# Optimization experiments

Measured on AMD Instinct MI355X. Metric: run time of the kernel, lower is better.

Reference implementation:

```python
import math
import jax, jax.numpy as jnp
import numpy as np

TOPK = 10
GAMMA = 0.0
DELTA = 0.05
EPS = 1e-8
QR_RANK_EPS = 1e-6
B, D, C = 4096, 2048, 10000


def setup_inputs() -> dict:
    key = jax.random.key(0)
    kz, kw, kn = jax.random.split(key, 3)
    z = jax.random.normal(kz, (B, D), jnp.float32)
    W = jax.random.normal(kw, (C, D), jnp.float32) * 0.02
    logits = z @ W.T                      # (B, C)
    y = jnp.argmax(logits, axis=1)        # correct-class labels -> positive margins
    noise = jax.random.normal(kn, (B, D), jnp.float32)  # one Gaussian draw per sample
    return {"z": z, "y": y, "logits": logits, "W": W, "noise": noise}


def reference(z, y, logits, W, noise):
    # z: (B,D), y: (B,), logits: (B,C), W: (C,D), noise: (B,D)
    b, d = z.shape
    c = W.shape[0]
    k = min(TOPK, c - 1)
    log_term = math.log(1.0 / max(DELTA, 1e-12))

    # top-K confusing classes (exclude true class)
    lm = logits.at[jnp.arange(b), y].set(-1e9)
    _, topk_idx = jax.lax.top_k(lm, k)            # (B, K)

    w_y = W[y]                                    # (B, D)
    w_ks = W[topk_idx]                            # (B, K, D)
    A = w_y[:, None, :] - w_ks                    # (B, K, D) rows = w_y - w_k

    # batched reduced QR of A^T : Q (B,D,K), R (B,K,K)
    Q, R = jnp.linalg.qr(jnp.swapaxes(A, 1, 2))
    keep = jnp.abs(jnp.diagonal(R, axis1=-2, axis2=-1)) > QR_RANK_EPS  # (B, K)
    Qm = Q * keep[:, None, :].astype(Q.dtype)     # zero dropped columns == Q[:, keep]
    valid_basis = keep.any(axis=1)

    # margins and nuisance-projected differences
    margins = jnp.einsum('bkd,bd->bk', A, z)                      # (B, K)
    coef = jnp.einsum('bkd,bdr->bkr', A, Qm)                      # (B, K, K)
    diffs_N = A - jnp.einsum('bkr,bdr->bkd', coef, Qm)            # (B, K, D)
    pn2 = jnp.maximum(jnp.sum(diffs_N * diffs_N, axis=-1), EPS)   # (B, K)
    slack = jnp.maximum(margins - GAMMA, 0.0)
    alpha_k = slack * slack / (2.0 * pn2 * log_term + EPS)
    alpha = jnp.min(alpha_k, axis=1)                              # (B,)

    valid = valid_basis & (alpha > 0.0) & jnp.isfinite(alpha)
    scale = jnp.where(valid, jnp.sqrt(jnp.maximum(alpha, 0.0)), 0.0)

    # project noise onto nuisance subspace and inject
    nc = jnp.einsum('bd,bdr->br', noise, Qm)
    epsN = noise - jnp.einsum('br,bdr->bd', nc, Qm)               # (B, D)
    z_aug = z + jax.lax.stop_gradient(scale[:, None] * epsN)
    # invalid samples carry scale=0 (z_aug == z); `valid` marks real augmentations
    return z_aug, y, valid
```

## Files before the change

### kernel.cpp

```cpp
#include <hip/hip_runtime.h>
#include <math.h>

#define BB 4096
#define DD 2048
#define CC 10000
#define KK 10
#define NT 256
#define NW 4
#define NF4 2500
#define TRI(k) ((k)*((k)+1)/2)

constexpr int PJ[55] = {0, 0,1, 0,1,2, 0,1,2,3, 0,1,2,3,4, 0,1,2,3,4,5,
                        0,1,2,3,4,5,6, 0,1,2,3,4,5,6,7, 0,1,2,3,4,5,6,7,8,
                        0,1,2,3,4,5,6,7,8,9};
constexpr int PK[55] = {0, 1,1, 2,2,2, 3,3,3,3, 4,4,4,4,4, 5,5,5,5,5,5,
                        6,6,6,6,6,6,6, 7,7,7,7,7,7,7,7, 8,8,8,8,8,8,8,8,8,
                        9,9,9,9,9,9,9,9,9,9};

__global__ __launch_bounds__(NT, 6) void topk_kernel(
    const float* __restrict__ logits, const int* __restrict__ y,
    int* __restrict__ topk)
{
    __shared__ float s_cv[NW * KK];
    __shared__ int   s_ci[NW * KK];

    const int b = blockIdx.x, tid = threadIdx.x;
    const int lane = tid & 63, wave = tid >> 6;
    const int yb = y[b];

    float4 lg[10];
    const float4* lrow = (const float4*)(logits + (size_t)b * CC);
    #pragma unroll
    for (int j = 0; j < 10; ++j) {
        const int i4 = tid + 256 * j;
        if (i4 < NF4) lg[j] = lrow[i4];
        else          lg[j] = make_float4(-3e38f, -3e38f, -3e38f, -3e38f);
    }
    #pragma unroll
    for (int j = 0; j < 10; ++j) {
        const int rel = yb - 4 * (tid + 256 * j);
        if (rel == 0) lg[j].x = -3e38f;
        else if (rel == 1) lg[j].y = -3e38f;
        else if (rel == 2) lg[j].z = -3e38f;
        else if (rel == 3) lg[j].w = -3e38f;
    }

    float lbest; int lbidx;
    auto rescan = [&]() {
        lbest = -3.1e38f; lbidx = 0x7fffffff;
        #pragma unroll
        for (int j = 0; j < 10; ++j) {
            const int base = 4 * (tid + 256 * j);
            if (lg[j].x > lbest) { lbest = lg[j].x; lbidx = base + 0; }
            if (lg[j].y > lbest) { lbest = lg[j].y; lbidx = base + 1; }
            if (lg[j].z > lbest) { lbest = lg[j].z; lbidx = base + 2; }
            if (lg[j].w > lbest) { lbest = lg[j].w; lbidx = base + 3; }
        }
    };
    rescan();

    for (int r = 0; r < KK; ++r) {
        float bv = lbest; int bi = lbidx;
        #pragma unroll
        for (int off = 32; off > 0; off >>= 1) {
            const float ov = __shfl_down(bv, off, 64);
            const int   oi = __shfl_down(bi, off, 64);
            if (ov > bv || (ov == bv && oi < bi)) { bv = ov; bi = oi; }
        }
        bv = __shfl(bv, 0, 64);
        bi = __shfl(bi, 0, 64);
        if (lane == 0) { s_cv[wave * KK + r] = bv; s_ci[wave * KK + r] = bi; }
        if (lbidx == bi) {
            const int jw = ((bi >> 2) - tid) >> 8;
            const int cw = bi & 3;
            #pragma unroll
            for (int j = 0; j < 10; ++j) if (j == jw) {
                if (cw == 0) lg[j].x = -3e38f;
                else if (cw == 1) lg[j].y = -3e38f;
                else if (cw == 2) lg[j].z = -3e38f;
                else lg[j].w = -3e38f;
            }
            rescan();
        }
    }
    __syncthreads();

    if (wave == 0) {
        float cv = (lane < NW * KK) ? s_cv[lane] : -3.1e38f;
        int   ci = (lane < NW * KK) ? s_ci[lane] : 0x7fffffff;
        for (int r = 0; r < KK; ++r) {
            float bv = cv; int bi = ci;
            #pragma unroll
            for (int off = 32; off > 0; off >>= 1) {
                const float ov = __shfl_down(bv, off, 64);
                const int   oi = __shfl_down(bi, off, 64);
                if (ov > bv || (ov == bv && oi < bi)) { bv = ov; bi = oi; }
            }
            bi = __shfl(bi, 0, 64);
            if (lane == 0) topk[b * KK + r] = bi;
            if (ci == bi) cv = -3.1e38f;
        }
    }
}

template<int LO, int CNT, int NROW, bool WZN>
__device__ __forceinline__ void pass1_accum(
    const float* __restrict__ W, const float* __restrict__ z,
    const float* __restrict__ noise, size_t wyo, size_t zoff,
    const int* kidx, int lane, float* s_g)
{
    float acc[CNT];
    #pragma unroll
    for (int t = 0; t < CNT; ++t) acc[t] = 0.0f;

    #pragma unroll 1
    for (int it = 0; it < 8; ++it) {
        const int p = lane + (it << 6);
        const float4 wy4 = ((const float4*)(W + wyo))[p];
        float4 a4[NROW];
        #pragma unroll
        for (int k = 0; k < NROW; ++k) {
            const float4 wk4 = ((const float4*)(W + (size_t)kidx[k] * DD))[p];
            a4[k].x = wy4.x - wk4.x; a4[k].y = wy4.y - wk4.y;
            a4[k].z = wy4.z - wk4.z; a4[k].w = wy4.w - wk4.w;
        }
        float4 z4 = make_float4(0.f, 0.f, 0.f, 0.f), n4 = z4;
        if (WZN) {
            z4 = ((const float4*)(z + zoff))[p];
            n4 = ((const float4*)(noise + zoff))[p];
        }
        #pragma unroll
        for (int e = 0; e < 4; ++e) {
            float ak[NROW];
            #pragma unroll
            for (int k = 0; k < NROW; ++k)
                ak[k] = (e == 0) ? a4[k].x : (e == 1) ? a4[k].y
                      : (e == 2) ? a4[k].z : a4[k].w;
            const float ze = (e == 0) ? z4.x : (e == 1) ? z4.y : (e == 2) ? z4.z : z4.w;
            const float ne = (e == 0) ? n4.x : (e == 1) ? n4.y : (e == 2) ? n4.z : n4.w;
            #pragma unroll
            for (int t = 0; t < CNT; ++t) {
                const int g = LO + t;
                if (g < 55)      acc[t] += ak[PJ[g < 55 ? g : 0]] * ak[PK[g < 55 ? g : 0]];
                else if (g < 65) acc[t] += ak[(g - 55) < NROW ? (g - 55) : 0] * ze;
                else             acc[t] += ak[(g - 65) < NROW ? (g - 65) : 0] * ne;
            }
        }
    }
    #pragma unroll
    for (int t = 0; t < CNT; ++t) {
        float x = acc[t];
        #pragma unroll
        for (int off = 32; off > 0; off >>= 1) x += __shfl_down(x, off, 64);
        if (lane == 0) s_g[LO + t] = x;
    }
}

__global__ __launch_bounds__(NT, 4) void aug_kernel(
    const float* __restrict__ z, const int* __restrict__ y,
    const float* __restrict__ W, const float* __restrict__ noise,
    const int* __restrict__ topk, float* __restrict__ out, int write_tail)
{
    __shared__ float s_g[80];
    __shared__ float s_sol[16];

    const int b = blockIdx.x, tid = threadIdx.x;
    const int lane = tid & 63, wave = tid >> 6;
    const int yb = y[b];

    int kidx[KK];
    #pragma unroll
    for (int k = 0; k < KK; ++k) kidx[k] = topk[b * KK + k];

    const size_t zoff = (size_t)b * DD;
    const size_t wyo  = (size_t)yb * DD;

    if (wave == 0)      pass1_accum< 0, 19,  6, false>(W, z, noise, wyo, zoff, kidx, lane, s_g);
    else if (wave == 1) pass1_accum<19, 19,  9, false>(W, z, noise, wyo, zoff, kidx, lane, s_g);
    else if (wave == 2) pass1_accum<38, 17, 10, false>(W, z, noise, wyo, zoff, kidx, lane, s_g);
    else                pass1_accum<55, 20, 10, true >(W, z, noise, wyo, zoff, kidx, lane, s_g);
    __syncthreads();

    if (wave == 0) {
        float g[75];
        #pragma unroll
        for (int t = 0; t < 75; ++t) g[t] = s_g[t];

        float dinv[KK];
        unsigned keepmask = 0u;
        #pragma unroll
        for (int k = 0; k < KK; ++k) {
            float s = g[TRI(k) + k];
            #pragma unroll
            for (int j = 0; j < KK; ++j) if (j < k) { const float l = g[TRI(k) + j]; s -= l * l; }
            const float dkk = sqrtf(fmaxf(s, 0.0f));
            const bool kp = dkk > 1e-6f;
            if (kp) keepmask |= (1u << k);
            dinv[k] = kp ? 1.0f / dkk : 0.0f;
            g[TRI(k) + k] = dkk;
            #pragma unroll
            for (int i = 0; i < KK; ++i) if (i > k) {
                float t2 = g[TRI(i) + k];
                #pragma unroll
                for (int j = 0; j < KK; ++j) if (j < k) t2 -= g[TRI(i) + j] * g[TRI(k) + j];
                g[TRI(i) + k] = t2 * dinv[k];
            }
        }
        float cvec[KK];
        #pragma unroll
        for (int i = 0; i < KK; ++i) {
            float s = g[65 + i];
            #pragma unroll
            for (int j = 0; j < KK; ++j) if (j < i) s -= g[TRI(i) + j] * cvec[j];
            cvec[i] = s * dinv[i];
        }
        #pragma unroll
        for (int i = KK - 1; i >= 0; --i) {
            float s = cvec[i];
            #pragma unroll
            for (int j = 0; j < KK; ++j) if (j > i) s -= g[TRI(j) + i] * cvec[j];
            cvec[i] = s * dinv[i];
        }
        const float denomf = 6.9914645e-8f;
        float amin = 3.0e38f;
        #pragma unroll
        for (int k = 0; k < KK; ++k) {
            const float sl = fmaxf(g[55 + k], 0.0f);
            amin = fminf(amin, sl * sl / denomf);
        }
        const bool valid = (keepmask != 0u) && (amin > 0.0f) && isfinite(amin);
        const float scale = valid ? sqrtf(amin) : 0.0f;
        if (lane == 0) {
            #pragma unroll
            for (int k = 0; k < KK; ++k) s_sol[k] = cvec[k];
            s_sol[10] = scale;
            s_sol[11] = valid ? 1.0f : 0.0f;
        }
    }
    __syncthreads();

    float cvec[KK];
    #pragma unroll
    for (int k = 0; k < KK; ++k) cvec[k] = s_sol[k];
    const float scale = s_sol[10];

    #pragma unroll
    for (int c = 0; c < 2; ++c) {
        const size_t coff = (size_t)c * 1024;
        const float4 wy4 = ((const float4*)(W + wyo + coff))[tid];
        float4 proj = make_float4(0.f, 0.f, 0.f, 0.f);
        float csum = 0.f;
        #pragma unroll
        for (int k = 0; k < KK; ++k) {
            const float4 wk4 = ((const float4*)(W + (size_t)kidx[k] * DD + coff))[tid];
            proj.x -= cvec[k] * wk4.x; proj.y -= cvec[k] * wk4.y;
            proj.z -= cvec[k] * wk4.z; proj.w -= cvec[k] * wk4.w;
            csum += cvec[k];
        }
        proj.x += csum * wy4.x; proj.y += csum * wy4.y;
        proj.z += csum * wy4.z; proj.w += csum * wy4.w;
        const float4 zc = ((const float4*)(z + zoff + coff))[tid];
        const float4 nc = ((const float4*)(noise + zoff + coff))[tid];
        float4 o;
        o.x = zc.x + scale * (nc.x - proj.x);
        o.y = zc.y + scale * (nc.y - proj.y);
        o.z = zc.z + scale * (nc.z - proj.z);
        o.w = zc.w + scale * (nc.w - proj.w);
        ((float4*)(out + zoff + coff))[tid] = o;
    }

    if (write_tail && tid == 0) {
        out[(size_t)BB * DD + b] = (float)yb;
        out[(size_t)BB * DD + BB + b] = s_sol[11];
    }
}

extern "C" void kernel_launch(void* const* d_in, const int* in_sizes, int n_in,
                              void* d_out, int out_size, void* d_ws, size_t ws_size,
                              hipStream_t stream) {
    const float* z      = (const float*)d_in[0];
    const int*   y      = (const int*)d_in[1];
    const float* logits = (const float*)d_in[2];
    const float* W      = (const float*)d_in[3];
    const float* noise  = (const float*)d_in[4];
    float* out = (float*)d_out;
    int* topk = (int*)d_ws;

    topk_kernel<<<BB, NT, 0, stream>>>(logits, y, topk);
    const int write_tail = (out_size >= BB * DD + 2 * BB) ? 1 : 0;
    aug_kernel<<<BB, NT, 0, stream>>>(z, y, W, noise, topk, out, write_tail);
}
```

Baseline: 455.4 us.

## Stage gathered W rows in LDS via global_load_lds shared across waves

Previously each of the four waves separately loaded the true-class row and up to ten top-k rows of W from global memory for its share of the Gram and margin accumulation. Now the block loads each 256-column chunk of the eleven rows into LDS once, using direct global-to-LDS loads spread across waves, and every wave reads its rows from LDS. This removes the redundant global/L2 gather traffic. It adds two block barriers per chunk and an 11 KB LDS buffer, and the launch-bounds occupancy hint is raised from 4 to 5.

```diff
diff --git a/kernel.cpp b/kernel.cpp
--- a/kernel.cpp
+++ b/kernel.cpp
@@ -9,6 +9,8 @@
 #define NW 4
 #define NF4 2500
 #define TRI(k) ((k)*((k)+1)/2)
+#define CH 256
+#define NCH (DD / CH)
 
 constexpr int PJ[55] = {0, 0,1, 0,1,2, 0,1,2,3, 0,1,2,3,4, 0,1,2,3,4,5,
                         0,1,2,3,4,5,6, 0,1,2,3,4,5,6,7, 0,1,2,3,4,5,6,7,8,
@@ -16,6 +18,12 @@
 constexpr int PK[55] = {0, 1,1, 2,2,2, 3,3,3,3, 4,4,4,4,4, 5,5,5,5,5,5,
                         6,6,6,6,6,6,6, 7,7,7,7,7,7,7,7, 8,8,8,8,8,8,8,8,8,
                         9,9,9,9,9,9,9,9,9,9};
+
+typedef __attribute__((address_space(3))) void       lds_void;
+typedef const __attribute__((address_space(1))) void gbl_cvoid;
+__device__ __forceinline__ void gll16(const float* gp, float* lp) {
+    __builtin_amdgcn_global_load_lds((gbl_cvoid*)gp, (lds_void*)lp, 16, 0, 0);
+}
 
 __global__ __launch_bounds__(NT, 6) void topk_kernel(
     const float* __restrict__ logits, const int* __restrict__ y,
@@ -104,30 +112,37 @@
 }
 
 template<int LO, int CNT, int NROW, bool WZN>
-__device__ __forceinline__ void pass1_accum(
+__device__ __forceinline__ void pass1(
     const float* __restrict__ W, const float* __restrict__ z,
-    const float* __restrict__ noise, size_t wyo, size_t zoff,
-    const int* kidx, int lane, float* s_g)
+    const float* __restrict__ noise, size_t zoff,
+    size_t rb0, size_t rb1, size_t rb2, int has2,
+    float* lp0, float* lp1, float* lp2,
+    int lane, float* s_w, float* s_g)
 {
     float acc[CNT];
     #pragma unroll
     for (int t = 0; t < CNT; ++t) acc[t] = 0.0f;
 
-    #pragma unroll 1
-    for (int it = 0; it < 8; ++it) {
-        const int p = lane + (it << 6);
-        const float4 wy4 = ((const float4*)(W + wyo))[p];
+    for (int c = 0; c < NCH; ++c) {
+        const int col = (c << 8) + (lane << 2);
+        gll16(W + rb0 + col, lp0);
+        gll16(W + rb1 + col, lp1);
+        if (has2) gll16(W + rb2 + col, lp2);
+        __syncthreads();
+
+        const float4* sw4 = (const float4*)s_w;
+        const float4 wy4 = sw4[(10 << 6) + lane];
         float4 a4[NROW];
         #pragma unroll
         for (int k = 0; k < NROW; ++k) {
-            const float4 wk4 = ((const float4*)(W + (size_t)kidx[k] * DD))[p];
+            const float4 wk4 = sw4[(k << 6) + lane];
             a4[k].x = wy4.x - wk4.x; a4[k].y = wy4.y - wk4.y;
             a4[k].z = wy4.z - wk4.z; a4[k].w = wy4.w - wk4.w;
         }
         float4 z4 = make_float4(0.f, 0.f, 0.f, 0.f), n4 = z4;
         if (WZN) {
-            z4 = ((const float4*)(z + zoff))[p];
-            n4 = ((const float4*)(noise + zoff))[p];
+            z4 = ((const float4*)(z + zoff))[(c << 6) + lane];
+            n4 = ((const float4*)(noise + zoff))[(c << 6) + lane];
         }
         #pragma unroll
         for (int e = 0; e < 4; ++e) {
@@ -146,6 +161,7 @@
                 else             acc[t] += ak[(g - 65) < NROW ? (g - 65) : 0] * ne;
             }
         }
+        __syncthreads();
     }
     #pragma unroll
     for (int t = 0; t < CNT; ++t) {
@@ -156,11 +172,12 @@
     }
 }
 
-__global__ __launch_bounds__(NT, 4) void aug_kernel(
+__global__ __launch_bounds__(NT, 5) void aug_kernel(
     const float* __restrict__ z, const int* __restrict__ y,
     const float* __restrict__ W, const float* __restrict__ noise,
     const int* __restrict__ topk, float* __restrict__ out, int write_tail)
 {
+    __shared__ __align__(16) float s_w[11 * CH];
     __shared__ float s_g[80];
     __shared__ float s_sol[16];
 
@@ -175,10 +192,19 @@
     const size_t zoff = (size_t)b * DD;
     const size_t wyo  = (size_t)yb * DD;
 
-    if (wave == 0)      pass1_accum< 0, 19,  6, false>(W, z, noise, wyo, zoff, kidx, lane, s_g);
-    else if (wave == 1) pass1_accum<19, 19,  9, false>(W, z, noise, wyo, zoff, kidx, lane, s_g);
-    else if (wave == 2) pass1_accum<38, 17, 10, false>(W, z, noise, wyo, zoff, kidx, lane, s_g);
-    else                pass1_accum<55, 20, 10, true >(W, z, noise, wyo, zoff, kidx, lane, s_g);
+    const size_t rb0 = (size_t)topk[b * KK + wave] * DD;
+    const size_t rb1 = (size_t)topk[b * KK + wave + 4] * DD;
+    const size_t rb2 = (wave == 2) ? wyo
+                     : (wave < 2) ? (size_t)topk[b * KK + wave + 8] * DD : 0;
+    const int has2 = (wave < 3) ? 1 : 0;
+    float* lp0 = s_w + wave * CH;
+    float* lp1 = s_w + (wave + 4) * CH;
+    float* lp2 = s_w + (wave + 8) * CH;
+
+    if (wave == 0)      pass1< 0, 19,  6, false>(W, z, noise, zoff, rb0, rb1, rb2, has2, lp0, lp1, lp2, lane, s_w, s_g);
+    else if (wave == 1) pass1<19, 19,  9, false>(W, z, noise, zoff, rb0, rb1, rb2, has2, lp0, lp1, lp2, lane, s_w, s_g);
+    else if (wave == 2) pass1<38, 17, 10, false>(W, z, noise, zoff, rb0, rb1, rb2, has2, lp0, lp1, lp2, lane, s_w, s_g);
+    else                pass1<55, 20, 10, true >(W, z, noise, zoff, rb0, rb1, rb2, has2, lp0, lp1, lp2, lane, s_w, s_g);
     __syncthreads();
 
     if (wave == 0) {
```

Result: slower. 1.652 ms (+262.6%).
